# Kernel optimization log

Measured on AMD Instinct MI355X. Metric: run time of the kernel, lower is better.

Reference implementation:

```python
import math
import jax, jax.numpy as jnp
import numpy as np

B, N, C = 2, 2048, 768
H, DH = 12, 64  # num_heads, head_dim


def setup_inputs() -> dict:
    key = jax.random.key(0)
    ks = jax.random.split(key, 5)
    s = 1.0 / math.sqrt(C)  # keep linear outputs O(1)
    return {
        "x": jax.random.normal(ks[0], (B, N, C), jnp.float32),
        "Wq": jax.random.normal(ks[1], (C, C), jnp.float32) * s,
        "bq": jnp.zeros((C,), jnp.float32),
        "Wk": jax.random.normal(ks[2], (C, C), jnp.float32) * s,
        "bk": jnp.zeros((C,), jnp.float32),
        "Wv": jax.random.normal(ks[3], (C, C), jnp.float32) * s,
        "bv": jnp.zeros((C,), jnp.float32),
        "Wp": jax.random.normal(ks[4], (C, C), jnp.float32) * s,
        "bp": jnp.zeros((C,), jnp.float32),
    }


def reference(x, Wq, bq, Wk, bk, Wv, bv, Wp, bp):
    # Linear projections; torch nn.Linear computes x @ W.T + b, here W stored
    # as (in, out) so it's x @ W + b with equivalent math.
    def split(t):  # [B,N,C] -> [B,H,N,DH]
        return t.reshape(B, N, H, DH).transpose(0, 2, 1, 3)

    q = split(x @ Wq + bq)
    k = split(x @ Wk + bk)
    v = split(x @ Wv + bv)
    scale = 1.0 / math.sqrt(DH)
    attn = jnp.einsum("bhqd,bhkd->bhqk", q, k) * scale  # [B,H,N,N]
    attn = jax.nn.softmax(attn, axis=-1)  # attn_drop=0.0 -> identity
    y = jnp.einsum("bhqk,bhkd->bhqd", attn, v)  # [B,H,N,DH]
    y = y.transpose(0, 2, 1, 3).reshape(B, N, C)
    return y @ Wp + bp  # proj_drop=0.0 -> identity
```

## Files before the change

kernel.cpp:

```cpp
#include <hip/hip_runtime.h>


typedef __bf16 bf16_t;
typedef __bf16 bf16x8 __attribute__((ext_vector_type(8)));
typedef __bf16 bf16x4 __attribute__((ext_vector_type(4)));
typedef float  floatx4 __attribute__((ext_vector_type(4)));
typedef unsigned int u32;

#define MFMA32(a, b, c) __builtin_amdgcn_mfma_f32_16x16x32_bf16(a, b, c, 0, 0, 0)

__device__ __forceinline__ void async16(const bf16_t* g, bf16_t* l) {
  __builtin_amdgcn_global_load_lds(
      (const __attribute__((address_space(1))) u32*)g,
      (__attribute__((address_space(3))) u32*)l, 16, 0, 0);
}

__global__ __launch_bounds__(256) void cvt_x_kernel(const float* __restrict__ x,
                                                    bf16_t* __restrict__ xb) {
  int i = blockIdx.x * 256 + threadIdx.x;
  floatx4 v = ((const floatx4*)x)[i];
  bf16x4 o;
  o[0] = (bf16_t)v[0]; o[1] = (bf16_t)v[1]; o[2] = (bf16_t)v[2]; o[3] = (bf16_t)v[3];
  ((bf16x4*)xb)[i] = o;
}

__global__ __launch_bounds__(256) void cvt_wt_kernel(
    const float* __restrict__ W0, const float* __restrict__ W1,
    const float* __restrict__ W2, const float* __restrict__ W3,
    bf16_t* __restrict__ T0, bf16_t* __restrict__ T1,
    bf16_t* __restrict__ T2, bf16_t* __restrict__ T3) {
  const int z = blockIdx.z;
  const float* W = (z == 0) ? W0 : (z == 1) ? W1 : (z == 2) ? W2 : W3;
  bf16_t* WT = (z == 0) ? T0 : (z == 1) ? T1 : (z == 2) ? T2 : T3;
  __shared__ bf16_t T[64][65];
  const int c = threadIdx.x & 63, r0 = threadIdx.x >> 6;
#pragma unroll
  for (int p = 0; p < 16; ++p) {
    int r = p * 4 + r0;
    T[r][c] = (bf16_t)W[(blockIdx.y * 64 + r) * 768 + blockIdx.x * 64 + c];
  }
  __syncthreads();
#pragma unroll
  for (int p = 0; p < 16; ++p) {
    int r = p * 4 + r0;
    WT[(blockIdx.x * 64 + r) * 768 + blockIdx.y * 64 + c] = T[c][r];
  }
}



__global__ __launch_bounds__(256) void gemm_qkv(
    const bf16_t* __restrict__ Xb, const bf16_t* __restrict__ WqT,
    const bf16_t* __restrict__ WkT, const bf16_t* __restrict__ WvT,
    const float* __restrict__ bq, const float* __restrict__ bk,
    const float* __restrict__ bv, bf16_t* __restrict__ qw,
    bf16_t* __restrict__ kw, bf16_t* __restrict__ vtw) {
  __shared__ bf16_t Al[128 * 64];
  __shared__ bf16_t Bl[128 * 64];
  const int z = blockIdx.z;
  const bf16_t* Wt = (z == 0) ? WqT : (z == 1) ? WkT : WvT;
  const float* bias = (z == 0) ? bq : (z == 1) ? bk : bv;
  const float oscale = (z == 0) ? 0.18033688011112042f : 1.0f;

  const int tid = threadIdx.x, lane = tid & 63, w = tid >> 6;
  const int wr = w >> 1, wc = w & 1;
  const int l15 = lane & 15, quad = lane >> 4;
  const int xr = l15 & 7;
  const int m0 = blockIdx.y * 128, n0 = blockIdx.x * 128;

  floatx4 acc[4][4] = {};

  for (int kt = 0; kt < 768; kt += 64) {
#pragma unroll
    for (int p = 0; p < 4; ++p) {
      const int cb = (p * 4 + w) * 64;
      const int c = cb + lane;
      const int r = c >> 3, j = (c & 7) ^ (r & 7);
      async16(&Wt[(m0 + r) * 768 + kt + j * 8], &Al[cb * 8]);
      async16(&Xb[(n0 + r) * 768 + kt + j * 8], &Bl[cb * 8]);
    }
    __syncthreads();
#pragma unroll
    for (int kk = 0; kk < 2; ++kk) {
      bf16x8 af[4], bfr[4];
#pragma unroll
      for (int i = 0; i < 4; ++i) {
        const int sl = ((kk * 4 + quad) ^ xr) * 8;
        af[i]  = *(bf16x8*)&Al[(wr * 64 + i * 16 + l15) * 64 + sl];
        bfr[i] = *(bf16x8*)&Bl[(wc * 64 + i * 16 + l15) * 64 + sl];
      }
#pragma unroll
      for (int mi = 0; mi < 4; ++mi)
#pragma unroll
        for (int ni = 0; ni < 4; ++ni)
          acc[mi][ni] = MFMA32(af[mi], bfr[ni], acc[mi][ni]);
    }
    __syncthreads();
  }

  const int hh = (m0 + wr * 64) >> 6;
#pragma unroll
  for (int mi = 0; mi < 4; ++mi) {
    const int d0 = mi * 16 + quad * 4;
    const int gm0 = m0 + wr * 64 + d0;
    float bv4[4];
#pragma unroll
    for (int r = 0; r < 4; ++r) bv4[r] = bias[gm0 + r];
#pragma unroll
    for (int ni = 0; ni < 4; ++ni) {
      const int gn = n0 + wc * 64 + ni * 16 + l15;
      const int bb = gn >> 11, tok = gn & 2047;
      const int bh = bb * 12 + hh;
      if (z == 0) {
        bf16x4 pk;
#pragma unroll
        for (int r = 0; r < 4; ++r)
          pk[r] = (bf16_t)((acc[mi][ni][r] + bv4[r]) * oscale);
        *(bf16x4*)&qw[bh * 131072 + tok * 64 + d0] = pk;
      } else if (z == 1) {
        const int kt2 = tok >> 7, k128 = tok & 127;
        const int nk = k128 >> 4, kl15 = k128 & 15;
        const int kk = d0 >> 5, kq = (d0 >> 3) & 3, j0 = d0 & 7;
        bf16x4 pk;
#pragma unroll
        for (int r = 0; r < 4; ++r)
          pk[r] = (bf16_t)(acc[mi][ni][r] + bv4[r]);
        *(bf16x4*)&kw[bh * 131072 + kt2 * 8192 +
                      ((nk * 2 + kk) * 64 + kq * 16 + kl15) * 8 + j0] = pk;
      } else {
        const int kt2 = tok >> 7, k128 = tok & 127;
        const int g = k128 >> 5, o = k128 & 31;
        const int qv = (o & 15) >> 2, jv = (o & 3) + ((o & 16) >> 2);
        const int base = bh * 131072 + kt2 * 8192 +
                         ((g * 4 + mi) * 64 + qv * 16 + quad * 4) * 8 + jv;
#pragma unroll
        for (int r = 0; r < 4; ++r)
          vtw[base + r * 8] = (bf16_t)(acc[mi][ni][r] + bv4[r]);
      }
    }
  }
}

__global__ __launch_bounds__(256) void gemm_proj(
    const bf16_t* __restrict__ Yb, const bf16_t* __restrict__ WpT,
    const float* __restrict__ bias, float* __restrict__ out) {
  __shared__ bf16_t Al[128 * 64];
  __shared__ bf16_t Bl[128 * 64];
  const int tid = threadIdx.x, lane = tid & 63, w = tid >> 6;
  const int wr = w >> 1, wc = w & 1;
  const int l15 = lane & 15, quad = lane >> 4;
  const int xr = l15 & 7;
  const int m0 = blockIdx.y * 128, n0 = blockIdx.x * 128;

  floatx4 acc[4][4] = {};

  for (int kt = 0; kt < 768; kt += 64) {
#pragma unroll
    for (int p = 0; p < 4; ++p) {
      const int cb = (p * 4 + w) * 64;
      const int c = cb + lane;
      const int r = c >> 3, j = (c & 7) ^ (r & 7);
      async16(&WpT[(m0 + r) * 768 + kt + j * 8], &Al[cb * 8]);
      async16(&Yb[(n0 + r) * 768 + kt + j * 8], &Bl[cb * 8]);
    }
    __syncthreads();
#pragma unroll
    for (int kk = 0; kk < 2; ++kk) {
      bf16x8 af[4], bfr[4];
#pragma unroll
      for (int i = 0; i < 4; ++i) {
        const int sl = ((kk * 4 + quad) ^ xr) * 8;
        af[i]  = *(bf16x8*)&Al[(wr * 64 + i * 16 + l15) * 64 + sl];
        bfr[i] = *(bf16x8*)&Bl[(wc * 64 + i * 16 + l15) * 64 + sl];
      }
#pragma unroll
      for (int mi = 0; mi < 4; ++mi)
#pragma unroll
        for (int ni = 0; ni < 4; ++ni)
          acc[mi][ni] = MFMA32(af[mi], bfr[ni], acc[mi][ni]);
    }
    __syncthreads();
  }

#pragma unroll
  for (int mi = 0; mi < 4; ++mi) {
    const int gm0 = m0 + wr * 64 + mi * 16 + quad * 4;
    floatx4 bv4;
#pragma unroll
    for (int r = 0; r < 4; ++r) bv4[r] = bias[gm0 + r];
#pragma unroll
    for (int ni = 0; ni < 4; ++ni) {
      const int gn = n0 + wc * 64 + ni * 16 + l15;
      floatx4 v = acc[mi][ni] + bv4;
      *(floatx4*)&out[gn * 768 + gm0] = v;
    }
  }
}

__global__ __launch_bounds__(512, 4) void attn_kernel(
    const bf16_t* __restrict__ Q, const bf16_t* __restrict__ Kf,
    const bf16_t* __restrict__ Vf, bf16_t* __restrict__ Y) {
  __shared__ __align__(16) float Ox[8][2][2][64][4];
  __shared__ float Ls[4][2][2][16];

  const int tid = threadIdx.x, lane = tid & 63, w = tid >> 6;
  const int wq = w & 1, wk = w >> 1;
  const int l15 = lane & 15, quad = lane >> 4;
  const int bh = blockIdx.y;
  const int q0 = blockIdx.x * 64;
  const bf16_t* Qb = Q + bh * 131072;
  const bf16_t* Kb = Kf + bh * 131072;
  const bf16_t* Vb = Vf + bh * 131072;

  bf16x8 qf[2][2];
#pragma unroll
  for (int ni = 0; ni < 2; ++ni)
#pragma unroll
    for (int kk = 0; kk < 2; ++kk)
      qf[ni][kk] = *(const bf16x8*)&Qb[(q0 + wq * 32 + ni * 16 + l15) * 64 +
                                       kk * 32 + quad * 8];

  floatx4 oacc[2][4] = {};
  float lsum[2] = {0.f, 0.f};

  for (int kt = 0; kt < 16; ++kt) {
    const bf16_t* kg = Kb + kt * 8192;
    const bf16_t* vg = Vb + kt * 8192;

    bf16x8 kfr[2][2];
#pragma unroll
    for (int mt = 0; mt < 2; ++mt)
#pragma unroll
      for (int kk = 0; kk < 2; ++kk)
        kfr[mt][kk] = *(const bf16x8*)&kg[((wk * 2 + mt) * 2 + kk) * 512 + lane * 8];

    floatx4 s[2][2] = {};
#pragma unroll
    for (int mt = 0; mt < 2; ++mt)
#pragma unroll
      for (int kk = 0; kk < 2; ++kk)
#pragma unroll
        for (int ni = 0; ni < 2; ++ni)
          s[mt][ni] = MFMA32(kfr[mt][kk], qf[ni][kk], s[mt][ni]);

    bf16x8 pk[2];
#pragma unroll
    for (int mt = 0; mt < 2; ++mt)
#pragma unroll
      for (int ni = 0; ni < 2; ++ni)
#pragma unroll
        for (int r = 0; r < 4; ++r) {
          const float pv = __builtin_amdgcn_exp2f(s[mt][ni][r]);
          lsum[ni] += pv;
          pk[ni][mt * 4 + r] = (bf16_t)pv;
        }

#pragma unroll
    for (int nd = 0; nd < 4; ++nd) {
      bf16x8 vfr = *(const bf16x8*)&vg[((wk * 4 + nd) * 64 + lane) * 8];
#pragma unroll
      for (int ni = 0; ni < 2; ++ni)
        oacc[ni][nd] = MFMA32(pk[ni], vfr, oacc[ni][nd]);
    }
  }

#pragma unroll
  for (int ni = 0; ni < 2; ++ni) {
    lsum[ni] += __shfl_xor(lsum[ni], 16);
    lsum[ni] += __shfl_xor(lsum[ni], 32);
  }
  if (quad == 0) {
#pragma unroll
    for (int ni = 0; ni < 2; ++ni) Ls[wk][wq][ni][l15] = lsum[ni];
  }

  const int h = wk & 1;
  const int sub = wk >> 1;

#pragma unroll
  for (int ni = 0; ni < 2; ++ni)
#pragma unroll
    for (int nd = 0; nd < 4; ++nd)
      if ((nd >> 1) != h)
        *(floatx4*)&Ox[w ^ 2][ni][nd & 1][lane][0] = oacc[ni][nd];
  __syncthreads();
#pragma unroll
  for (int ni = 0; ni < 2; ++ni)
#pragma unroll
    for (int nd = 0; nd < 4; ++nd)
      if ((nd >> 1) == h)
        oacc[ni][nd] += *(floatx4*)&Ox[w][ni][nd & 1][lane][0];

  float tot[2][4];
#pragma unroll
  for (int ni = 0; ni < 2; ++ni)
#pragma unroll
    for (int r = 0; r < 4; ++r)
      tot[ni][r] = Ls[0][wq][ni][quad * 4 + r] + Ls[1][wq][ni][quad * 4 + r] +
                   Ls[2][wq][ni][quad * 4 + r] + Ls[3][wq][ni][quad * 4 + r];
  __syncthreads();

#pragma unroll
  for (int ni = 0; ni < 2; ++ni)
#pragma unroll
    for (int nd = 0; nd < 4; ++nd)
      if ((nd >> 1) == h && (nd & 1) != sub)
        *(floatx4*)&Ox[w ^ 4][ni][0][lane][0] = oacc[ni][nd];
  __syncthreads();

  const int bb = bh / 12, hh = bh % 12;
  const int nd_own = 2 * h + sub;
#pragma unroll
  for (int ni = 0; ni < 2; ++ni) {
    floatx4 o = {};
#pragma unroll
    for (int nd = 0; nd < 4; ++nd)
      if ((nd >> 1) == h && (nd & 1) == sub) o = oacc[ni][nd];
    o += *(floatx4*)&Ox[w][ni][0][lane][0];
    const int col = hh * 64 + nd_own * 16 + l15;
#pragma unroll
    for (int r = 0; r < 4; ++r) {
      const int tok = q0 + wq * 32 + ni * 16 + quad * 4 + r;
      Y[(bb * 2048 + tok) * 768 + col] = (bf16_t)(o[r] / tot[ni][r]);
    }
  }
}

extern "C" void kernel_launch(void* const* d_in, const int* in_sizes, int n_in,
                              void* d_out, int out_size, void* d_ws, size_t ws_size,
                              hipStream_t stream) {
  const float* x  = (const float*)d_in[0];
  const float* Wq = (const float*)d_in[1];
  const float* bq = (const float*)d_in[2];
  const float* Wk = (const float*)d_in[3];
  const float* bk = (const float*)d_in[4];
  const float* Wv = (const float*)d_in[5];
  const float* bv = (const float*)d_in[6];
  const float* Wp = (const float*)d_in[7];
  const float* bp = (const float*)d_in[8];
  float* out = (float*)d_out;

  char* ws = (char*)d_ws;
  bf16_t* xb  = (bf16_t*)ws; ws += (size_t)4096 * 768 * 2;
  bf16_t* WqT = (bf16_t*)ws; ws += (size_t)768 * 768 * 2;
  bf16_t* WkT = (bf16_t*)ws; ws += (size_t)768 * 768 * 2;
  bf16_t* WvT = (bf16_t*)ws; ws += (size_t)768 * 768 * 2;
  bf16_t* WpT = (bf16_t*)ws; ws += (size_t)768 * 768 * 2;
  bf16_t* qw  = (bf16_t*)ws; ws += (size_t)24 * 2048 * 64 * 2;
  bf16_t* kw  = (bf16_t*)ws; ws += (size_t)24 * 2048 * 64 * 2;
  bf16_t* vtw = (bf16_t*)ws; ws += (size_t)24 * 2048 * 64 * 2;
  bf16_t* yw  = (bf16_t*)ws; ws += (size_t)4096 * 768 * 2;

  cvt_x_kernel<<<3072, 256, 0, stream>>>(x, xb);
  cvt_wt_kernel<<<dim3(12, 12, 4), 256, 0, stream>>>(Wq, Wk, Wv, Wp, WqT, WkT, WvT, WpT);

  gemm_qkv<<<dim3(32, 6, 3), 256, 0, stream>>>(xb, WqT, WkT, WvT, bq, bk, bv, qw, kw, vtw);
  attn_kernel<<<dim3(32, 24), 512, 0, stream>>>(qw, kw, vtw, yw);
  gemm_proj<<<dim3(32, 6), 256, 0, stream>>>(yw, WpT, bp, out);
}
```

Baseline: 193.7 us.

## Merge conversion kernels and double-buffer K fragments in attention loop

Fuses the x conversion and weight-transpose kernels into a single launch to remove one kernel launch and its tail. In the attention kernel, K fragments for the next tile are prefetched into alternating register buffers, and V loads are issued before the QK MFMAs so global load latency overlaps compute. This raises register pressure and may lower occupancy.

After: 193.2 us. No clear change (-0.3%).

```diff
diff --git a/kernel.cpp b/kernel.cpp
--- a/kernel.cpp
+++ b/kernel.cpp
@@ -15,21 +15,23 @@
       (__attribute__((address_space(3))) u32*)l, 16, 0, 0);
 }
 
-__global__ __launch_bounds__(256) void cvt_x_kernel(const float* __restrict__ x,
-                                                    bf16_t* __restrict__ xb) {
-  int i = blockIdx.x * 256 + threadIdx.x;
-  floatx4 v = ((const floatx4*)x)[i];
-  bf16x4 o;
-  o[0] = (bf16_t)v[0]; o[1] = (bf16_t)v[1]; o[2] = (bf16_t)v[2]; o[3] = (bf16_t)v[3];
-  ((bf16x4*)xb)[i] = o;
-}
-
-__global__ __launch_bounds__(256) void cvt_wt_kernel(
+__global__ __launch_bounds__(256) void cvt_all(
+    const float* __restrict__ x, bf16_t* __restrict__ xb,
     const float* __restrict__ W0, const float* __restrict__ W1,
     const float* __restrict__ W2, const float* __restrict__ W3,
     bf16_t* __restrict__ T0, bf16_t* __restrict__ T1,
     bf16_t* __restrict__ T2, bf16_t* __restrict__ T3) {
-  const int z = blockIdx.z;
+  if (blockIdx.x < 3072) {
+    int i = blockIdx.x * 256 + threadIdx.x;
+    floatx4 v = ((const floatx4*)x)[i];
+    bf16x4 o;
+    o[0] = (bf16_t)v[0]; o[1] = (bf16_t)v[1]; o[2] = (bf16_t)v[2]; o[3] = (bf16_t)v[3];
+    ((bf16x4*)xb)[i] = o;
+    return;
+  }
+  const int b = blockIdx.x - 3072;
+  const int z = b / 144, rem = b % 144;
+  const int by = rem / 12, bx = rem % 12;
   const float* W = (z == 0) ? W0 : (z == 1) ? W1 : (z == 2) ? W2 : W3;
   bf16_t* WT = (z == 0) ? T0 : (z == 1) ? T1 : (z == 2) ? T2 : T3;
   __shared__ bf16_t T[64][65];
@@ -37,13 +39,13 @@
 #pragma unroll
   for (int p = 0; p < 16; ++p) {
     int r = p * 4 + r0;
-    T[r][c] = (bf16_t)W[(blockIdx.y * 64 + r) * 768 + blockIdx.x * 64 + c];
+    T[r][c] = (bf16_t)W[(by * 64 + r) * 768 + bx * 64 + c];
   }
   __syncthreads();
 #pragma unroll
   for (int p = 0; p < 16; ++p) {
     int r = p * 4 + r0;
-    WT[(blockIdx.x * 64 + r) * 768 + blockIdx.y * 64 + c] = T[c][r];
+    WT[(bx * 64 + r) * 768 + by * 64 + c] = T[c][r];
   }
 }
 
@@ -223,44 +225,68 @@
   floatx4 oacc[2][4] = {};
   float lsum[2] = {0.f, 0.f};
 
-  for (int kt = 0; kt < 16; ++kt) {
-    const bf16_t* kg = Kb + kt * 8192;
-    const bf16_t* vg = Vb + kt * 8192;
-
-    bf16x8 kfr[2][2];
-#pragma unroll
-    for (int mt = 0; mt < 2; ++mt)
-#pragma unroll
-      for (int kk = 0; kk < 2; ++kk)
-        kfr[mt][kk] = *(const bf16x8*)&kg[((wk * 2 + mt) * 2 + kk) * 512 + lane * 8];
-
-    floatx4 s[2][2] = {};
-#pragma unroll
-    for (int mt = 0; mt < 2; ++mt)
-#pragma unroll
-      for (int kk = 0; kk < 2; ++kk)
+  const int kfo = (wk * 2) * 1024 + lane * 8;
+  const int vfo = (wk * 4) * 512 + lane * 8;
+
+  bf16x8 kA[2][2], kB[2][2];
+#pragma unroll
+  for (int mt = 0; mt < 2; ++mt)
+#pragma unroll
+    for (int kk = 0; kk < 2; ++kk)
+      kA[mt][kk] = *(const bf16x8*)&Kb[kfo + mt * 1024 + kk * 512];
+
+#pragma unroll 1
+  for (int kt2 = 0; kt2 < 8; ++kt2) {
+#pragma unroll
+    for (int half = 0; half < 2; ++half) {
+      const int kt = kt2 * 2 + half;
+      const bf16_t* vg = Vb + kt * 8192;
+      const bf16_t* kgn = Kb + ((kt + 1) & 15) * 8192;
+
+      bf16x8 vfr[4];
+#pragma unroll
+      for (int nd = 0; nd < 4; ++nd)
+        vfr[nd] = *(const bf16x8*)&vg[vfo + nd * 512];
+      if (half == 0) {
+#pragma unroll
+        for (int mt = 0; mt < 2; ++mt)
+#pragma unroll
+          for (int kk = 0; kk < 2; ++kk)
+            kB[mt][kk] = *(const bf16x8*)&kgn[kfo + mt * 1024 + kk * 512];
+      } else {
+#pragma unroll
+        for (int mt = 0; mt < 2; ++mt)
+#pragma unroll
+          for (int kk = 0; kk < 2; ++kk)
+            kA[mt][kk] = *(const bf16x8*)&kgn[kfo + mt * 1024 + kk * 512];
+      }
+
+      bf16x8 pk[2];
+#pragma unroll
+      for (int mt = 0; mt < 2; ++mt) {
+        floatx4 s[2] = {};
+#pragma unroll
+        for (int kk = 0; kk < 2; ++kk) {
+          const bf16x8 kfr = (half == 0) ? kA[mt][kk] : kB[mt][kk];
+#pragma unroll
+          for (int ni = 0; ni < 2; ++ni)
+            s[ni] = MFMA32(kfr, qf[ni][kk], s[ni]);
+        }
 #pragma unroll
         for (int ni = 0; ni < 2; ++ni)
-          s[mt][ni] = MFMA32(kfr[mt][kk], qf[ni][kk], s[mt][ni]);
-
-    bf16x8 pk[2];
-#pragma unroll
-    for (int mt = 0; mt < 2; ++mt)
-#pragma unroll
-      for (int ni = 0; ni < 2; ++ni)
-#pragma unroll
-        for (int r = 0; r < 4; ++r) {
-          const float pv = __builtin_amdgcn_exp2f(s[mt][ni][r]);
-          lsum[ni] += pv;
-          pk[ni][mt * 4 + r] = (bf16_t)pv;
-        }
-
-#pragma unroll
-    for (int nd = 0; nd < 4; ++nd) {
-      bf16x8 vfr = *(const bf16x8*)&vg[((wk * 4 + nd) * 64 + lane) * 8];
-#pragma unroll
-      for (int ni = 0; ni < 2; ++ni)
-        oacc[ni][nd] = MFMA32(pk[ni], vfr, oacc[ni][nd]);
+#pragma unroll
+          for (int r = 0; r < 4; ++r) {
+            const float pv = __builtin_amdgcn_exp2f(s[ni][r]);
+            lsum[ni] += pv;
+            pk[ni][mt * 4 + r] = (bf16_t)pv;
+          }
+      }
+
+#pragma unroll
+      for (int nd = 0; nd < 4; ++nd)
+#pragma unroll
+        for (int ni = 0; ni < 2; ++ni)
+          oacc[ni][nd] = MFMA32(pk[ni], vfr[nd], oacc[ni][nd]);
     }
   }
 
@@ -351,9 +377,7 @@
   bf16_t* vtw = (bf16_t*)ws; ws += (size_t)24 * 2048 * 64 * 2;
   bf16_t* yw  = (bf16_t*)ws; ws += (size_t)4096 * 768 * 2;
 
-  cvt_x_kernel<<<3072, 256, 0, stream>>>(x, xb);
-  cvt_wt_kernel<<<dim3(12, 12, 4), 256, 0, stream>>>(Wq, Wk, Wv, Wp, WqT, WkT, WvT, WpT);
-
+  cvt_all<<<3648, 256, 0, stream>>>(x, xb, Wq, Wk, Wv, Wp, WqT, WkT, WvT, WpT);
   gemm_qkv<<<dim3(32, 6, 3), 256, 0, stream>>>(xb, WqT, WkT, WvT, bq, bk, bv, qw, kw, vtw);
   attn_kernel<<<dim3(32, 24), 512, 0, stream>>>(qw, kw, vtw, yw);
   gemm_proj<<<dim3(32, 6), 256, 0, stream>>>(yw, WpT, bp, out);
```
